# Kernel tuning notes

Hardware: AMD Instinct MI355X
Metric: run time of the kernel (lower is better)

The kernel has to match this reference:

```python
import jax, jax.numpy as jnp
import numpy as np

NOT_EPSILON = 1.0
B, Q, K, T = 2, 512, 512, 256  # batch, num queries, num keys, dims


def swishmax(x, axis):
    # x * exp(x - max) / (sum(|x * exp(x - max)|) + 1)
    xexp = x * jnp.exp(x - jnp.max(x, axis=axis, keepdims=True))
    return xexp / (jnp.sum(jnp.abs(xexp), axis=axis, keepdims=True) + NOT_EPSILON)


def setup_inputs() -> dict:
    key = jax.random.key(0)
    ks = jax.random.split(key, 8)
    s = 1.0 / np.sqrt(T)
    return {
        "query_tokens": jax.random.normal(ks[0], (B, Q, T), jnp.float32),
        "key_tokens": jax.random.normal(ks[1], (B, K, T), jnp.float32),
        "value_tokens": jax.random.normal(ks[2], (B, K, T), jnp.float32),
        "Wk": jax.random.normal(ks[3], (T, T), jnp.float32) * s,
        "Wq": jax.random.normal(ks[4], (T, T), jnp.float32) * s,
        "Wva": jax.random.normal(ks[5], (T, T), jnp.float32) * s,
        "Wal": jax.random.normal(ks[6], (T, T), jnp.float32) * s,
        "Wvo": jax.random.normal(ks[7], (T, T), jnp.float32) * s,
    }


def reference(query_tokens, key_tokens, value_tokens, Wk, Wq, Wva, Wal, Wvo):
    # torch nn.Linear: y = x @ W.T (no biases)
    k = jnp.einsum('bkt,ut->bku', key_tokens, Wk)      # [B,K,T]
    q = jnp.einsum('bqt,ut->bqu', query_tokens, Wq)    # [B,Q,T]
    # elementwise outer product over token pairs: [B,K,Q,T]
    raw = k[:, :, None, :] * q[:, None, :, :]
    logits = jnp.einsum('bkqt,ut->bkqu', raw, Wal)     # [B,K,Q,T]
    scale = swishmax(logits, axis=-2)                  # normalize over Q
    v = jnp.einsum('bkt,ut->bku', value_tokens, Wva)   # [B,K,T]
    values_scaled = v[:, :, None, :] * scale           # [B,K,Q,T]
    value_sum = values_scaled.sum(axis=-3)             # sum over K -> [B,Q,T]
    return jnp.einsum('bqt,ut->bqu', value_sum, Wvo)   # [B,Q,T]
```

## Files before the change

### kernel.cpp

```cpp
#include <hip/hip_runtime.h>
#include <cstdint>


typedef short bf16x8 __attribute__((ext_vector_type(8)));
typedef float f32x4  __attribute__((ext_vector_type(4)));

__device__ inline float bf2f(short s) {
  return __uint_as_float(((unsigned)(unsigned short)s) << 16);
}
__device__ inline unsigned packrn(float lo, float hi) {
  return __builtin_amdgcn_perm(__float_as_uint(hi) + 0x8000u,
                               __float_as_uint(lo) + 0x8000u, 0x07060302u);
}
__device__ inline unsigned encM(float f) {
  unsigned k = (unsigned)__float_as_int(f);
  return (k & 0x80000000u) ? ~k : (k | 0x80000000u);
}
__device__ inline float decM(unsigned k) {
  int i = (k & 0x80000000u) ? (int)(k ^ 0x80000000u) : (int)~k;
  return __int_as_float(i);
}

#define FMA16()                                                                 \
  c[0][0] += a.x*w.x; c[0][1] += a.x*w.y; c[0][2] += a.x*w.z; c[0][3] += a.x*w.w; \
  c[1][0] += a.y*w.x; c[1][1] += a.y*w.y; c[1][2] += a.y*w.z; c[1][3] += a.y*w.w; \
  c[2][0] += a.z*w.x; c[2][1] += a.z*w.y; c[2][2] += a.z*w.z; c[2][3] += a.z*w.w; \
  c[3][0] += a.w*w.x; c[3][1] += a.w*w.y; c[3][2] += a.w*w.z; c[3][3] += a.w*w.w;

#define GEMM_BODY_RM(X, W)                                                      \
  __shared__ __align__(16) float As[16][68];                                    \
  __shared__ __align__(16) float Ws[16][68];                                    \
  const int tid = threadIdx.x;                                                  \
  const int tx4 = (tid & 15) * 4;                                               \
  const int ty4 = (tid >> 4) * 4;                                               \
  const int m0 = blockIdx.x * 64, u0 = blockIdx.y * 64;                         \
  const int lmi = tid >> 2, lc4 = (tid & 3) * 4;                                \
  float c[4][4] = {};                                                           \
  _Pragma("unroll 1")                                                           \
  for (int t0 = 0; t0 < 256; t0 += 16) {                                        \
    const float4 xa = *(const float4*)&(X)[(size_t)(m0 + lmi) * 256 + t0 + lc4];\
    const float4 wb = *(const float4*)&(W)[(size_t)(u0 + lmi) * 256 + t0 + lc4];\
    __syncthreads();                                                            \
    As[lc4 + 0][lmi] = xa.x; As[lc4 + 1][lmi] = xa.y;                           \
    As[lc4 + 2][lmi] = xa.z; As[lc4 + 3][lmi] = xa.w;                           \
    Ws[lc4 + 0][lmi] = wb.x; Ws[lc4 + 1][lmi] = wb.y;                           \
    Ws[lc4 + 2][lmi] = wb.z; Ws[lc4 + 3][lmi] = wb.w;                           \
    __syncthreads();                                                            \
    _Pragma("unroll")                                                           \
    for (int t = 0; t < 16; ++t) {                                              \
      const float4 a = *(const float4*)&As[t][ty4];                             \
      const float4 w = *(const float4*)&Ws[t][tx4];                             \
      FMA16();                                                                  \
    }                                                                           \
  }

__global__ __launch_bounds__(256) void proj3(
    const float* __restrict__ key, const float* __restrict__ value,
    const float* __restrict__ query, const float* __restrict__ Wk,
    const float* __restrict__ Wq, const float* __restrict__ Wva,
    const float* __restrict__ Wal, float* __restrict__ kproj,
    float* __restrict__ vproj, short* __restrict__ qpF,
    short* __restrict__ WalF, float* __restrict__ vsum)
{
  const int z = blockIdx.z;
  if (z == 3) {
    const int p = blockIdx.x * 4 + blockIdx.y;
    const int t256 = threadIdx.x;
#pragma unroll
    for (int e = 0; e < 4; ++e) {
      const int d = p * 1024 + t256 * 4 + e;
      const int j = d & 7, uu = (d >> 3) & 31, c8g = d >> 8;
      const int ucx = c8g >> 5, cc = c8g & 31;
      const float v = Wal[(ucx * 32 + uu) * 256 + cc * 8 + j];
      WalF[d] = (short)packrn(v, v);
    }
    float4* vz = (float4*)(vsum + p * 4096);
#pragma unroll
    for (int e = 0; e < 4; ++e) vz[t256 * 4 + e] = make_float4(0.f, 0.f, 0.f, 0.f);
    return;
  }
  const float* X = (z == 0) ? key : (z == 1) ? value : query;
  const float* W = (z == 0) ? Wk  : (z == 1) ? Wva   : Wq;
  GEMM_BODY_RM(X, W);
  if (z == 2) {
    const int tbase = u0 + tx4;
    const int ks = tbase >> 5, l4f = (tbase & 31) >> 3, j0 = tbase & 7;
#pragma unroll
    for (int i = 0; i < 4; ++i) {
      const int m = m0 + ty4 + i;
      const int bb = m >> 9, q = m & 511;
      const int g = q >> 4, l15q = q & 15;
      const size_t idx = ((size_t)(((bb * 32 + g) * 8 + ks) * 64) + l4f * 16 + l15q) * 8 + j0;
      uint2 s; s.x = packrn(c[i][0], c[i][1]); s.y = packrn(c[i][2], c[i][3]);
      *(uint2*)&qpF[idx] = s;
    }
  } else {
    float* C = (z == 0) ? kproj : vproj;
#pragma unroll
    for (int i = 0; i < 4; ++i)
      *(float4*)&C[(size_t)(m0 + ty4 + i) * 256 + u0 + tx4] =
          make_float4(c[i][0], c[i][1], c[i][2], c[i][3]);
  }
}

__global__ __launch_bounds__(256) void gemm_out(
    const float* __restrict__ X, const float* __restrict__ W, float* __restrict__ out)
{
  GEMM_BODY_RM(X, W);
#pragma unroll
  for (int i = 0; i < 4; ++i)
    *(float4*)&out[(size_t)(m0 + ty4 + i) * 256 + u0 + tx4] =
        make_float4(c[i][0], c[i][1], c[i][2], c[i][3]);
}

union Frag { bf16x8 v; unsigned u[4]; };

__global__ __launch_bounds__(512, 2) void kernelC(
    const short* __restrict__ qpF, const float* __restrict__ kproj,
    const float* __restrict__ vproj, const short* __restrict__ WalF,
    float* __restrict__ vsum)
{
  __shared__ __align__(16) short W2F[2][8192];
  __shared__ float vpS[32 * 33];
  __shared__ unsigned statM[96];
  __shared__ float statS[96];

  const int kt = blockIdx.x, uc = blockIdx.y, b = blockIdx.z;
  const int u0 = uc * 32, k0 = kt * 32;
  const int tid = threadIdx.x;
  const int lane = tid & 63, w = tid >> 6;
  const int l15 = lane & 15, l4 = lane >> 4;
  const int uu = tid & 31, c8 = tid >> 5;

  if (tid < 96) { statM[tid] = 0u; statS[tid] = 0.f; }
  {
    const int kk = tid >> 4, uu2 = (tid & 15) * 2;
    const float2 v2 = *(const float2*)&vproj[(size_t)(b * 512 + k0 + kk) * 256 + u0 + uu2];
    vpS[kk * 33 + uu2] = v2.x; vpS[kk * 33 + uu2 + 1] = v2.y;
  }

  float wl0[8], wl1[8];
  {
    const bf16x8 w0 = *(const bf16x8*)&WalF[((size_t)(uc * 32 + c8) * 32 + uu) * 8];
    const bf16x8 w1 = *(const bf16x8*)&WalF[((size_t)(uc * 32 + c8 + 16) * 32 + uu) * 8];
#pragma unroll
    for (int j = 0; j < 8; ++j) { wl0[j] = bf2f(w0[j]); wl1[j] = bf2f(w1[j]); }
  }

  const short* qbase = qpF + (size_t)b * 131072;
  Frag qa[4][8];
#pragma unroll
  for (int qg = 0; qg < 4; ++qg)
#pragma unroll
    for (int ks = 0; ks < 8; ++ks) {
      qa[qg][ks].v = *(const bf16x8*)&qbase[(((size_t)(w * 4 + qg) * 8 + ks) * 64 + lane) * 8];
      asm volatile("" : "+v"(qa[qg][ks].u[0]), "+v"(qa[qg][ks].u[1]),
                        "+v"(qa[qg][ks].u[2]), "+v"(qa[qg][ks].u[3]));
    }

  {
    const long krow = (long)(b * 512 + k0) * 256;
    const f32x4 a0 = *(const f32x4*)&kproj[krow + c8 * 8];
    const f32x4 a1 = *(const f32x4*)&kproj[krow + c8 * 8 + 4];
    const f32x4 b0 = *(const f32x4*)&kproj[krow + (c8 + 16) * 8];
    const f32x4 b1 = *(const f32x4*)&kproj[krow + (c8 + 16) * 8 + 4];
    uint4 st;
    st.x = packrn(wl0[0] * a0[0], wl0[1] * a0[1]);
    st.y = packrn(wl0[2] * a0[2], wl0[3] * a0[3]);
    st.z = packrn(wl0[4] * a1[0], wl0[5] * a1[1]);
    st.w = packrn(wl0[6] * a1[2], wl0[7] * a1[3]);
    *(uint4*)&W2F[0][(c8 * 32 + uu) * 8] = st;
    st.x = packrn(wl1[0] * b0[0], wl1[1] * b0[1]);
    st.y = packrn(wl1[2] * b0[2], wl1[3] * b0[3]);
    st.z = packrn(wl1[4] * b1[0], wl1[5] * b1[1]);
    st.w = packrn(wl1[6] * b1[2], wl1[7] * b1[3]);
    *(uint4*)&W2F[0][((c8 + 16) * 32 + uu) * 8] = st;
  }
  __syncthreads();

  const f32x4 z4 = {0.f, 0.f, 0.f, 0.f};
  f32x4 acc[4][2] = {z4, z4, z4, z4, z4, z4, z4, z4};

#pragma unroll 1
  for (int kk = 0; kk < 32; ++kk) {
    const int cs = kk & 1, ss = kk % 3;

    f32x4 a0, a1, b0, b1;
    if (kk < 31) {
      const long krn = (long)(b * 512 + k0 + kk + 1) * 256;
      a0 = *(const f32x4*)&kproj[krn + c8 * 8];
      a1 = *(const f32x4*)&kproj[krn + c8 * 8 + 4];
      b0 = *(const f32x4*)&kproj[krn + (c8 + 16) * 8];
      b1 = *(const f32x4*)&kproj[krn + (c8 + 16) * 8 + 4];
    }

    f32x4 lg[4][2] = {z4, z4, z4, z4, z4, z4, z4, z4};
#pragma unroll
    for (int ks = 0; ks < 8; ++ks) {
      const bf16x8 f0 = *(const bf16x8*)&W2F[cs][((ks * 4 + l4) * 32 + l15) * 8];
      const bf16x8 f1 = *(const bf16x8*)&W2F[cs][((ks * 4 + l4) * 32 + 16 + l15) * 8];
#pragma unroll
      for (int qg = 0; qg < 4; ++qg) {
        lg[qg][0] = __builtin_amdgcn_mfma_f32_16x16x32_bf16(qa[qg][ks].v, f0, lg[qg][0], 0, 0, 0);
        lg[qg][1] = __builtin_amdgcn_mfma_f32_16x16x32_bf16(qa[qg][ks].v, f1, lg[qg][1], 0, 0, 0);
      }
    }

    if (kk < 31) {
      uint4 st;
      st.x = packrn(wl0[0] * a0[0], wl0[1] * a0[1]);
      st.y = packrn(wl0[2] * a0[2], wl0[3] * a0[3]);
      st.z = packrn(wl0[4] * a1[0], wl0[5] * a1[1]);
      st.w = packrn(wl0[6] * a1[2], wl0[7] * a1[3]);
      *(uint4*)&W2F[cs ^ 1][(c8 * 32 + uu) * 8] = st;
      st.x = packrn(wl1[0] * b0[0], wl1[1] * b0[1]);
      st.y = packrn(wl1[2] * b0[2], wl1[3] * b0[3]);
      st.z = packrn(wl1[4] * b1[0], wl1[5] * b1[1]);
      st.w = packrn(wl1[6] * b1[2], wl1[7] * b1[3]);
      *(uint4*)&W2F[cs ^ 1][((c8 + 16) * 32 + uu) * 8] = st;
    }

    float Mv[2], Sv[2];
#pragma unroll
    for (int ug = 0; ug < 2; ++ug) {
      float m = lg[0][ug][0];
#pragma unroll
      for (int qg = 0; qg < 4; ++qg)
#pragma unroll
        for (int i = 0; i < 4; ++i) m = fmaxf(m, lg[qg][ug][i]);
      float s = 0.f;
#pragma unroll
      for (int qg = 0; qg < 4; ++qg)
#pragma unroll
        for (int i = 0; i < 4; ++i) {
          const float x = lg[qg][ug][i];
          const float p = x * __expf(x);
          lg[qg][ug][i] = p;
          s += fabsf(p);
        }
      m = fmaxf(m, __shfl_xor(m, 16));
      m = fmaxf(m, __shfl_xor(m, 32));
      s += __shfl_xor(s, 16);
      s += __shfl_xor(s, 32);
      Mv[ug] = m; Sv[ug] = s;
    }
    if (l4 == 0) {
      atomicMax(&statM[ss * 32 + l15],      encM(Mv[0]));
      atomicMax(&statM[ss * 32 + 16 + l15], encM(Mv[1]));
      atomicAdd(&statS[ss * 32 + l15],      Sv[0]);
      atomicAdd(&statS[ss * 32 + 16 + l15], Sv[1]);
    }
    __syncthreads();

#pragma unroll
    for (int ug = 0; ug < 2; ++ug) {
      const int ui = ug * 16 + l15;
      const float M = decM(statM[ss * 32 + ui]);
      const float S = statS[ss * 32 + ui];
      const float em = __expf(-M);
      const float g = vpS[kk * 33 + ui] * em / fmaf(S, em, 1.0f);
#pragma unroll
      for (int qg = 0; qg < 4; ++qg)
#pragma unroll
        for (int i = 0; i < 4; ++i)
          acc[qg][ug][i] = fmaf(g, lg[qg][ug][i], acc[qg][ug][i]);
    }
    const int rs = (kk + 2) % 3;
    if (tid < 32) { statM[rs * 32 + tid] = 0u; statS[rs * 32 + tid] = 0.f; }
  }

#pragma unroll
  for (int qg = 0; qg < 4; ++qg)
#pragma unroll
    for (int ug = 0; ug < 2; ++ug)
#pragma unroll
      for (int i = 0; i < 4; ++i)
        atomicAdd(&vsum[(size_t)(b * 512 + w * 64 + qg * 16 + l4 * 4 + i) * 256 +
                        u0 + ug * 16 + l15],
                  acc[qg][ug][i]);
}

extern "C" void kernel_launch(void* const* d_in, const int* in_sizes, int n_in,
                              void* d_out, int out_size, void* d_ws, size_t ws_size,
                              hipStream_t stream) {
  const float* query = (const float*)d_in[0];
  const float* key   = (const float*)d_in[1];
  const float* value = (const float*)d_in[2];
  const float* Wk    = (const float*)d_in[3];
  const float* Wq    = (const float*)d_in[4];
  const float* Wva   = (const float*)d_in[5];
  const float* Wal   = (const float*)d_in[6];
  const float* Wvo   = (const float*)d_in[7];
  float* ws = (float*)d_ws;

  float* kproj = ws;
  float* vproj = kproj + 262144;
  float* vsum  = vproj + 262144;
  short* qpF   = (short*)(vsum + 262144);
  short* WalF  = qpF + 262144;
  float* out   = (float*)d_out;

  proj3<<<dim3(16, 4, 4), 256, 0, stream>>>(key, value, query, Wk, Wq, Wva, Wal,
                                            kproj, vproj, qpF, WalF, vsum);
  kernelC<<<dim3(16, 8, 2), 512, 0, stream>>>(qpF, kproj, vproj, WalF, vsum);
  gemm_out<<<dim3(16, 4), 256, 0, stream>>>(vsum, Wvo, out);
}
```

Measured before the change: 197.0 us.

## Use 1024-thread blocks in kernelC with half the per-wave query tile

Doubles kernelC's block size from 512 to 1024 threads, so each of the 16 waves handles 32 queries instead of 64. Each thread now builds one W2F fragment instead of two, with fewer registers for q fragments and accumulators. The aim is more waves in flight to hide latency, and the per-step reciprocal division becomes a hardware rcp. The cost is heavier block-wide __syncthreads per k-step and more LDS atomic contention on the stats, with the same total MFMA work.

```diff
diff --git a/kernel.cpp b/kernel.cpp
--- a/kernel.cpp
+++ b/kernel.cpp
@@ -115,7 +115,7 @@
 
 union Frag { bf16x8 v; unsigned u[4]; };
 
-__global__ __launch_bounds__(512, 2) void kernelC(
+__global__ __launch_bounds__(1024, 4) void kernelC(
     const short* __restrict__ qpF, const float* __restrict__ kproj,
     const float* __restrict__ vproj, const short* __restrict__ WalF,
     float* __restrict__ vsum)
@@ -133,27 +133,22 @@
   const int uu = tid & 31, c8 = tid >> 5;
 
   if (tid < 96) { statM[tid] = 0u; statS[tid] = 0.f; }
-  {
-    const int kk = tid >> 4, uu2 = (tid & 15) * 2;
-    const float2 v2 = *(const float2*)&vproj[(size_t)(b * 512 + k0 + kk) * 256 + u0 + uu2];
-    vpS[kk * 33 + uu2] = v2.x; vpS[kk * 33 + uu2 + 1] = v2.y;
-  }
-
-  float wl0[8], wl1[8];
+  vpS[c8 * 33 + uu] = vproj[(size_t)(b * 512 + k0 + c8) * 256 + u0 + uu];
+
+  float wl[8];
   {
     const bf16x8 w0 = *(const bf16x8*)&WalF[((size_t)(uc * 32 + c8) * 32 + uu) * 8];
-    const bf16x8 w1 = *(const bf16x8*)&WalF[((size_t)(uc * 32 + c8 + 16) * 32 + uu) * 8];
-#pragma unroll
-    for (int j = 0; j < 8; ++j) { wl0[j] = bf2f(w0[j]); wl1[j] = bf2f(w1[j]); }
+#pragma unroll
+    for (int j = 0; j < 8; ++j) wl[j] = bf2f(w0[j]);
   }
 
   const short* qbase = qpF + (size_t)b * 131072;
-  Frag qa[4][8];
-#pragma unroll
-  for (int qg = 0; qg < 4; ++qg)
+  Frag qa[2][8];
+#pragma unroll
+  for (int qg = 0; qg < 2; ++qg)
 #pragma unroll
     for (int ks = 0; ks < 8; ++ks) {
-      qa[qg][ks].v = *(const bf16x8*)&qbase[(((size_t)(w * 4 + qg) * 8 + ks) * 64 + lane) * 8];
+      qa[qg][ks].v = *(const bf16x8*)&qbase[(((size_t)(w * 2 + qg) * 8 + ks) * 64 + lane) * 8];
       asm volatile("" : "+v"(qa[qg][ks].u[0]), "+v"(qa[qg][ks].u[1]),
                         "+v"(qa[qg][ks].u[2]), "+v"(qa[qg][ks].u[3]));
     }
@@ -162,45 +157,36 @@
     const long krow = (long)(b * 512 + k0) * 256;
     const f32x4 a0 = *(const f32x4*)&kproj[krow + c8 * 8];
     const f32x4 a1 = *(const f32x4*)&kproj[krow + c8 * 8 + 4];
-    const f32x4 b0 = *(const f32x4*)&kproj[krow + (c8 + 16) * 8];
-    const f32x4 b1 = *(const f32x4*)&kproj[krow + (c8 + 16) * 8 + 4];
     uint4 st;
-    st.x = packrn(wl0[0] * a0[0], wl0[1] * a0[1]);
-    st.y = packrn(wl0[2] * a0[2], wl0[3] * a0[3]);
-    st.z = packrn(wl0[4] * a1[0], wl0[5] * a1[1]);
-    st.w = packrn(wl0[6] * a1[2], wl0[7] * a1[3]);
+    st.x = packrn(wl[0] * a0[0], wl[1] * a0[1]);
+    st.y = packrn(wl[2] * a0[2], wl[3] * a0[3]);
+    st.z = packrn(wl[4] * a1[0], wl[5] * a1[1]);
+    st.w = packrn(wl[6] * a1[2], wl[7] * a1[3]);
     *(uint4*)&W2F[0][(c8 * 32 + uu) * 8] = st;
-    st.x = packrn(wl1[0] * b0[0], wl1[1] * b0[1]);
-    st.y = packrn(wl1[2] * b0[2], wl1[3] * b0[3]);
-    st.z = packrn(wl1[4] * b1[0], wl1[5] * b1[1]);
-    st.w = packrn(wl1[6] * b1[2], wl1[7] * b1[3]);
-    *(uint4*)&W2F[0][((c8 + 16) * 32 + uu) * 8] = st;
   }
   __syncthreads();
 
   const f32x4 z4 = {0.f, 0.f, 0.f, 0.f};
-  f32x4 acc[4][2] = {z4, z4, z4, z4, z4, z4, z4, z4};
+  f32x4 acc[2][2] = {z4, z4, z4, z4};
 
 #pragma unroll 1
   for (int kk = 0; kk < 32; ++kk) {
     const int cs = kk & 1, ss = kk % 3;
 
-    f32x4 a0, a1, b0, b1;
+    f32x4 a0, a1;
     if (kk < 31) {
       const long krn = (long)(b * 512 + k0 + kk + 1) * 256;
       a0 = *(const f32x4*)&kproj[krn + c8 * 8];
       a1 = *(const f32x4*)&kproj[krn + c8 * 8 + 4];
-      b0 = *(const f32x4*)&kproj[krn + (c8 + 16) * 8];
-      b1 = *(const f32x4*)&kproj[krn + (c8 + 16) * 8 + 4];
-    }
-
-    f32x4 lg[4][2] = {z4, z4, z4, z4, z4, z4, z4, z4};
+    }
+
+    f32x4 lg[2][2] = {z4, z4, z4, z4};
 #pragma unroll
     for (int ks = 0; ks < 8; ++ks) {
       const bf16x8 f0 = *(const bf16x8*)&W2F[cs][((ks * 4 + l4) * 32 + l15) * 8];
       const bf16x8 f1 = *(const bf16x8*)&W2F[cs][((ks * 4 + l4) * 32 + 16 + l15) * 8];
 #pragma unroll
-      for (int qg = 0; qg < 4; ++qg) {
+      for (int qg = 0; qg < 2; ++qg) {
         lg[qg][0] = __builtin_amdgcn_mfma_f32_16x16x32_bf16(qa[qg][ks].v, f0, lg[qg][0], 0, 0, 0);
         lg[qg][1] = __builtin_amdgcn_mfma_f32_16x16x32_bf16(qa[qg][ks].v, f1, lg[qg][1], 0, 0, 0);
       }
@@ -208,16 +194,11 @@
 
     if (kk < 31) {
       uint4 st;
-      st.x = packrn(wl0[0] * a0[0], wl0[1] * a0[1]);
-      st.y = packrn(wl0[2] * a0[2], wl0[3] * a0[3]);
-      st.z = packrn(wl0[4] * a1[0], wl0[5] * a1[1]);
-      st.w = packrn(wl0[6] * a1[2], wl0[7] * a1[3]);
+      st.x = packrn(wl[0] * a0[0], wl[1] * a0[1]);
+      st.y = packrn(wl[2] * a0[2], wl[3] * a0[3]);
+      st.z = packrn(wl[4] * a1[0], wl[5] * a1[1]);
+      st.w = packrn(wl[6] * a1[2], wl[7] * a1[3]);
       *(uint4*)&W2F[cs ^ 1][(c8 * 32 + uu) * 8] = st;
-      st.x = packrn(wl1[0] * b0[0], wl1[1] * b0[1]);
-      st.y = packrn(wl1[2] * b0[2], wl1[3] * b0[3]);
-      st.z = packrn(wl1[4] * b1[0], wl1[5] * b1[1]);
-      st.w = packrn(wl1[6] * b1[2], wl1[7] * b1[3]);
-      *(uint4*)&W2F[cs ^ 1][((c8 + 16) * 32 + uu) * 8] = st;
     }
 
     float Mv[2], Sv[2];
@@ -225,12 +206,12 @@
     for (int ug = 0; ug < 2; ++ug) {
       float m = lg[0][ug][0];
 #pragma unroll
-      for (int qg = 0; qg < 4; ++qg)
+      for (int qg = 0; qg < 2; ++qg)
 #pragma unroll
         for (int i = 0; i < 4; ++i) m = fmaxf(m, lg[qg][ug][i]);
       float s = 0.f;
 #pragma unroll
-      for (int qg = 0; qg < 4; ++qg)
+      for (int qg = 0; qg < 2; ++qg)
 #pragma unroll
         for (int i = 0; i < 4; ++i) {
           const float x = lg[qg][ug][i];
@@ -258,9 +239,9 @@
       const float M = decM(statM[ss * 32 + ui]);
       const float S = statS[ss * 32 + ui];
       const float em = __expf(-M);
-      const float g = vpS[kk * 33 + ui] * em / fmaf(S, em, 1.0f);
-#pragma unroll
-      for (int qg = 0; qg < 4; ++qg)
+      const float g = vpS[kk * 33 + ui] * em * __builtin_amdgcn_rcpf(fmaf(S, em, 1.0f));
+#pragma unroll
+      for (int qg = 0; qg < 2; ++qg)
 #pragma unroll
         for (int i = 0; i < 4; ++i)
           acc[qg][ug][i] = fmaf(g, lg[qg][ug][i], acc[qg][ug][i]);
@@ -270,12 +251,12 @@
   }
 
 #pragma unroll
-  for (int qg = 0; qg < 4; ++qg)
+  for (int qg = 0; qg < 2; ++qg)
 #pragma unroll
     for (int ug = 0; ug < 2; ++ug)
 #pragma unroll
       for (int i = 0; i < 4; ++i)
-        atomicAdd(&vsum[(size_t)(b * 512 + w * 64 + qg * 16 + l4 * 4 + i) * 256 +
+        atomicAdd(&vsum[(size_t)(b * 512 + w * 32 + qg * 16 + l4 * 4 + i) * 256 +
                         u0 + ug * 16 + l15],
                   acc[qg][ug][i]);
 }
@@ -302,6 +283,6 @@
 
   proj3<<<dim3(16, 4, 4), 256, 0, stream>>>(key, value, query, Wk, Wq, Wva, Wal,
                                             kproj, vproj, qpF, WalF, vsum);
-  kernelC<<<dim3(16, 8, 2), 512, 0, stream>>>(qpF, kproj, vproj, WalF, vsum);
+  kernelC<<<dim3(16, 8, 2), 1024, 0, stream>>>(qpF, kproj, vproj, WalF, vsum);
   gemm_out<<<dim3(16, 4), 256, 0, stream>>>(vsum, Wvo, out);
 }
```

After: 209.2 us. +6.2%, slower.
